# Kernel optimization log

Hardware: AMD Instinct MI355X
Metric: run time of the kernel (lower is better)

The kernel has to match this reference:

```python
import jax, jax.numpy as jnp
import numpy as np

N_NODES = 100000
N_EDGES = 3200000
IN_C, HID_C, OUT_C = 128, 64, 64


def setup_inputs() -> dict:
    key = jax.random.key(0)
    k = jax.random.split(key, 6)
    x = jax.random.normal(k[0], (N_NODES, IN_C), dtype=jnp.float32)
    edge_index = jax.random.randint(k[1], (2, N_EDGES), 0, N_NODES, dtype=jnp.int64)
    edge_weight = jax.random.uniform(k[2], (N_EDGES,), dtype=jnp.float32)
    W1 = jax.random.normal(k[3], (IN_C, HID_C), dtype=jnp.float32) * (1.0 / np.sqrt(IN_C))
    b1 = jnp.zeros((HID_C,), dtype=jnp.float32)
    W2 = jax.random.normal(k[4], (HID_C, OUT_C), dtype=jnp.float32) * (1.0 / np.sqrt(HID_C))
    b2 = jnp.zeros((OUT_C,), dtype=jnp.float32)
    return {"x": x, "edge_index": edge_index, "edge_weight": edge_weight,
            "W1": W1, "b1": b1, "W2": W2, "b2": b2}


def _gcn_norm(edge_index, edge_weight, num_nodes, dtype):
    # PyG GCNConv default: add self-loops (weight 1), symmetric normalization
    loop = jnp.arange(num_nodes, dtype=edge_index.dtype)
    row = jnp.concatenate([edge_index[0], loop])  # sources
    col = jnp.concatenate([edge_index[1], loop])  # targets (aggregation dim)
    w = jnp.concatenate([edge_weight.astype(dtype), jnp.ones((num_nodes,), dtype)])
    deg = jax.ops.segment_sum(w, col, num_segments=num_nodes)
    deg_inv_sqrt = jnp.where(deg > 0, jax.lax.rsqrt(deg), jnp.zeros((), dtype))
    norm = deg_inv_sqrt[row] * w * deg_inv_sqrt[col]
    return row, col, norm


def _gcn_conv(h, row, col, norm, W, b, num_nodes):
    h = h @ W                      # [N, C_out]
    msg = h[row] * norm[:, None]   # gather over sources, scale by edge norm
    out = jax.ops.segment_sum(msg, col, num_segments=num_nodes)  # scatter-add to targets
    return out + b


def reference(x, edge_index, edge_weight, W1, b1, W2, b2):
    num_nodes = x.shape[0]
    row, col, norm = _gcn_norm(edge_index, edge_weight, num_nodes, x.dtype)
    h = _gcn_conv(x, row, col, norm, W1, b1, num_nodes)
    h = jax.nn.relu(h)
    return _gcn_conv(h, row, col, norm, W2, b2, num_nodes)
```

## Files before the change

### kernel.cpp

```cpp
#include <hip/hip_runtime.h>
#include <hip/hip_bf16.h>

#define N_NODES 100000
#define N_EDGES 3200000
#define IN_C 128
#define HID_C 64
#define OUT_C 64

#define NBUCKET 196
#define SC_EDGES 4096
#define SC_PER   (SC_EDGES / 256)
#define SC_GRID  782
#define CAP 18432
#define MM1_GRID (N_NODES / 16)

struct EdgeRec { int s; float v; };

typedef float f32x2 __attribute__((ext_vector_type(2)));
typedef float f32x4 __attribute__((ext_vector_type(4)));
typedef short bf16x8 __attribute__((ext_vector_type(8)));
union F8 { uint4 u; bf16x8 f; };

__device__ __forceinline__ unsigned pack_bf16(float lo, float hi) {
    unsigned short l = __hip_bfloat16_raw(__float2bfloat16(lo)).x;
    unsigned short h = __hip_bfloat16_raw(__float2bfloat16(hi)).x;
    return ((unsigned)h << 16) | l;
}
__device__ __forceinline__ float bf_lo(unsigned u) {
    union { unsigned u; float f; } c; c.u = u << 16; return c.f;
}
__device__ __forceinline__ float bf_hi(unsigned u) {
    union { unsigned u; float f; } c; c.u = u & 0xffff0000u; return c.f;
}
__device__ __forceinline__ f32x2 bfp(unsigned u) {
    union { unsigned u; float f; } lo, hi;
    lo.u = u << 16; hi.u = u & 0xffff0000u;
    f32x2 r; r.x = lo.f; r.y = hi.f; return r;
}
__device__ __forceinline__ void pk_fma(f32x2& acc, f32x2 a, f32x2 w) {
    asm("v_pk_fma_f32 %0, %1, %2, %0" : "+v"(acc) : "v"(a), "v"(w));
}
__device__ __forceinline__ void edge_acc(f32x2* acc2, uint4 u, float w) {
    f32x2 wv; wv.x = w; wv.y = w;
    pk_fma(acc2[0], bfp(u.x), wv);
    pk_fma(acc2[1], bfp(u.y), wv);
    pk_fma(acc2[2], bfp(u.z), wv);
    pk_fma(acc2[3], bfp(u.w), wv);
}
__device__ __forceinline__ unsigned cvt_pk_bf16(float lo, float hi) {
    unsigned r;
    asm("v_cvt_pk_bf16_f32 %0, %1, %2" : "=v"(r) : "v"(lo), "v"(hi));
    return r;
}
__device__ __forceinline__ void split_frag(const float* f, uint4& hi4, uint4& lo4) {
    unsigned hi[4], lo[4];
    #pragma unroll
    for (int p = 0; p < 4; ++p) {
        hi[p] = cvt_pk_bf16(f[2 * p], f[2 * p + 1]);
        float r0 = f[2 * p]     - bf_lo(hi[p]);
        float r1 = f[2 * p + 1] - bf_hi(hi[p]);
        lo[p] = cvt_pk_bf16(r0, r1);
    }
    hi4 = make_uint4(hi[0], hi[1], hi[2], hi[3]);
    lo4 = make_uint4(lo[0], lo[1], lo[2], lo[3]);
}

__device__ __forceinline__ void scatter_body(const int* __restrict__ ei,
                                             const float* __restrict__ ew,
                                             int* __restrict__ gcursor,
                                             uint2* __restrict__ tmp,
                                             int* hist, int* scn, int* lcur,
                                             int* adj, uint2* rec,
                                             unsigned char* bk) {
    int tid = threadIdx.x;
    hist[tid] = 0;
    __syncthreads();
    int base = blockIdx.x * SC_EDGES;
    unsigned ys[SC_PER];
    float    ws[SC_PER];
    int      bs[SC_PER];
    for (int i = 0; i < SC_PER; ++i) {
        int e = base + i * 256 + tid;
        if (e < N_EDGES) {
            int t = ei[N_EDGES + e];
            bs[i] = t >> 9;
            ys[i] = (unsigned)ei[e] | ((unsigned)(t & 511) << 17);
            ws[i] = ew[e];
            atomicAdd(&hist[bs[i]], 1);
        } else bs[i] = -1;
    }
    __syncthreads();
    int v = hist[tid];
    scn[tid] = v;
    __syncthreads();
    for (int off = 1; off < 256; off <<= 1) {
        int t = scn[tid];
        int add = (tid >= off) ? scn[tid - off] : 0;
        __syncthreads();
        scn[tid] = t + add;
        __syncthreads();
    }
    int excl = scn[tid] - v;
    int gb = (v > 0) ? atomicAdd(&gcursor[tid], v) : 0;
    lcur[tid] = excl;
    adj[tid] = tid * CAP + gb - excl;
    __syncthreads();
    for (int i = 0; i < SC_PER; ++i) {
        if (bs[i] >= 0) {
            int j = atomicAdd(&lcur[bs[i]], 1);
            rec[j] = make_uint2(__float_as_uint(ws[i]), ys[i]);
            bk[j] = (unsigned char)bs[i];
        }
    }
    __syncthreads();
    int count = N_EDGES - base;
    if (count > SC_EDGES) count = SC_EDGES;
    for (int j = tid; j < count; j += 256) {
        int b = bk[j];
        tmp[adj[b] + j] = rec[j];
    }
}

template<int K>
__device__ __forceinline__ void mm_tile_bf(int tile,
                                           const float* __restrict__ X,
                                           const F8* bhi, const F8* blo,
                                           int lr, int kr, int col,
                                           unsigned* __restrict__ h) {
    constexpr int NKS = K / 32;
    int row0 = tile * 16;
    const float* xbase = X + (size_t)(row0 + lr) * K + kr * 8;
    float4 xa[NKS], xb[NKS];
    #pragma unroll
    for (int ks = 0; ks < NKS; ++ks) {
        const float4* xp = (const float4*)(xbase + ks * 32);
        xa[ks] = xp[0];
        xb[ks] = xp[1];
    }
    f32x4 acc = {0.f, 0.f, 0.f, 0.f};
    #pragma unroll
    for (int ks = 0; ks < NKS; ++ks) {
        float f[8] = {xa[ks].x, xa[ks].y, xa[ks].z, xa[ks].w,
                      xb[ks].x, xb[ks].y, xb[ks].z, xb[ks].w};
        F8 ahi, alo;
        split_frag(f, ahi.u, alo.u);
        acc = __builtin_amdgcn_mfma_f32_16x16x32_bf16(ahi.f, bhi[ks].f, acc, 0, 0, 0);
        acc = __builtin_amdgcn_mfma_f32_16x16x32_bf16(ahi.f, blo[ks].f, acc, 0, 0, 0);
        acc = __builtin_amdgcn_mfma_f32_16x16x32_bf16(alo.f, bhi[ks].f, acc, 0, 0, 0);
    }
    int rbase = row0 + kr * 4;
    float v0 = acc[0], v1 = acc[1], v2 = acc[2], v3 = acc[3];
    float o0 = __shfl_xor(v0, 1, 64);
    float o1 = __shfl_xor(v1, 1, 64);
    float o2 = __shfl_xor(v2, 1, 64);
    float o3 = __shfl_xor(v3, 1, 64);
    if ((lr & 1) == 0) {
        int ci = col >> 1;
        h[(rbase + 0) * 32 + ci] = pack_bf16(v0, o0);
        h[(rbase + 1) * 32 + ci] = pack_bf16(v1, o1);
        h[(rbase + 2) * 32 + ci] = pack_bf16(v2, o2);
        h[(rbase + 3) * 32 + ci] = pack_bf16(v3, o3);
    }
}

template<int K>
__device__ __forceinline__ void load_bfrags(const float* __restrict__ W,
                                            int kr, int col, F8* bhi, F8* blo) {
    #pragma unroll
    for (int ks = 0; ks < K / 32; ++ks) {
        const float* wp = W + (ks * 32 + kr * 8) * 64 + col;
        float f[8];
        #pragma unroll
        for (int j = 0; j < 8; ++j) f[j] = wp[j * 64];
        split_frag(f, bhi[ks].u, blo[ks].u);
    }
}

__global__ __launch_bounds__(256) void fused_scatter_mm1(const int* __restrict__ ei,
                                                         const float* __restrict__ ew,
                                                         int* __restrict__ gcursor,
                                                         uint2* __restrict__ tmp,
                                                         const float* __restrict__ x,
                                                         const float* __restrict__ W1,
                                                         unsigned* __restrict__ h) {
    __shared__ int hist[256];
    __shared__ int scn[256];
    __shared__ int lcur[256];
    __shared__ int adj[256];
    __shared__ uint2 rec[SC_EDGES];
    __shared__ unsigned char bk[SC_EDGES];
    if (blockIdx.x >= SC_GRID) {
        int l  = threadIdx.x & 63;
        int lr = l & 15;
        int kr = l >> 4;
        int col = (threadIdx.x >> 6) * 16 + lr;
        F8 bhi[IN_C / 32], blo[IN_C / 32];
        load_bfrags<IN_C>(W1, kr, col, bhi, blo);
        mm_tile_bf<IN_C>(blockIdx.x - SC_GRID, x, bhi, blo, lr, kr, col, h);
        return;
    }
    scatter_body(ei, ew, gcursor, tmp, hist, scn, lcur, adj, rec, bk);
}

template<int K>
__global__ __launch_bounds__(256) void mm_mfma_raw(const float* __restrict__ X,
                                                   const float* __restrict__ W,
                                                   unsigned* __restrict__ h) {
    int l  = threadIdx.x & 63;
    int lr = l & 15;
    int kr = l >> 4;
    int col = (threadIdx.x >> 6) * 16 + lr;
    F8 bhi[K / 32], blo[K / 32];
    load_bfrags<K>(W, kr, col, bhi, blo);
    for (int t = blockIdx.x; t < N_NODES / 16; t += gridDim.x)
        mm_tile_bf<K>(t, X, bhi, blo, lr, kr, col, h);
}

__global__ __launch_bounds__(512) void fine_sort(const int* __restrict__ gcursor,
                                                 const uint2* __restrict__ tmpPad,
                                                 int* __restrict__ rowptr,
                                                 float* __restrict__ dis,
                                                 EdgeRec* __restrict__ ed) {
    __shared__ int   cnt[512];
    __shared__ float wdeg[512];
    __shared__ int   s[512];
    __shared__ int   bsc[256];
    int tid = threadIdx.x;
    if (tid < 256) bsc[tid] = gcursor[tid];
    __syncthreads();
    for (int off = 1; off < 256; off <<= 1) {
        int t = (tid < 256) ? bsc[tid] : 0;
        int add = (tid < 256 && tid >= off) ? bsc[tid - off] : 0;
        __syncthreads();
        if (tid < 256) bsc[tid] = t + add;
        __syncthreads();
    }
    int bkt = blockIdx.x;
    int nEdge = gcursor[bkt];
    int bb = bsc[bkt] - nEdge;
    int nodeBase = bkt << 9;
    const uint2* tb = tmpPad + (size_t)bkt * CAP;
    cnt[tid] = 0;
    wdeg[tid] = 0.f;
    __syncthreads();
    for (int e = tid; e < nEdge; e += 512) {
        uint2 r = tb[e];
        int l = (r.y >> 17) & 511;
        atomicAdd(&cnt[l], 1);
        atomicAdd(&wdeg[l], __uint_as_float(r.x));
    }
    __syncthreads();
    int v = cnt[tid];
    s[tid] = v;
    __syncthreads();
    for (int off = 1; off < 512; off <<= 1) {
        int t = s[tid];
        int add = (tid >= off) ? s[tid - off] : 0;
        __syncthreads();
        s[tid] = t + add;
        __syncthreads();
    }
    int excl = s[tid] - v;
    int node = nodeBase + tid;
    if (node < N_NODES) {
        rowptr[node] = bb + excl;
        dis[node] = rsqrtf(wdeg[tid] + 1.0f);
    }
    if (node == N_NODES) rowptr[N_NODES] = N_EDGES;
    cnt[tid] = excl;
    __syncthreads();
    for (int e = tid; e < nEdge; e += 512) {
        uint2 r = tb[e];
        int l = (r.y >> 17) & 511;
        int p = atomicAdd(&cnt[l], 1);
        EdgeRec o;
        o.s = (int)(r.y & 0x1FFFFu);
        o.v = __uint_as_float(r.x);
        ed[bb + p] = o;
    }
}

__global__ __launch_bounds__(256, 8) void agg_kernel(const int* __restrict__ rowptr,
                                                     const EdgeRec* __restrict__ ed,
                                                     const unsigned* __restrict__ h,
                                                     const float* __restrict__ dis,
                                                     const float* __restrict__ b,
                                                     float* __restrict__ out,
                                                     int relu) {
    int node = blockIdx.x * 4 + (threadIdx.x >> 6);
    int lane = threadIdx.x & 63;
    int g = lane >> 3;
    int cl = lane & 7;
    int beg = rowptr[node];
    int end = rowptr[node + 1];
    const uint4* h16 = (const uint4*)h;
    const char*  hb  = (const char*)h + (size_t)cl * 16;
    float d  = dis[node];
    uint4 us = h16[(size_t)node * 8 + cl];
    f32x2 acc2[4];
    acc2[0] = 0.f; acc2[1] = 0.f; acc2[2] = 0.f; acc2[3] = 0.f;
    int n = end - beg;
    int nb = (n + 31) >> 5;
    int nm1 = n - 1;
    uint2 q0, q1, q2, q3;
    if (nb > 0) {
        q0 = *(const uint2*)(ed + beg + min(g,      nm1));
        q1 = *(const uint2*)(ed + beg + min(g + 8,  nm1));
        q2 = *(const uint2*)(ed + beg + min(g + 16, nm1));
        q3 = *(const uint2*)(ed + beg + min(g + 24, nm1));
        for (int bt = 0; bt < nb; ++bt) {
            int ob = (bt << 5) + g;
            float w0 = (ob      < n) ? __uint_as_float(q0.y) * dis[(int)q0.x] : 0.f;
            float w1 = (ob + 8  < n) ? __uint_as_float(q1.y) * dis[(int)q1.x] : 0.f;
            float w2 = (ob + 16 < n) ? __uint_as_float(q2.y) * dis[(int)q2.x] : 0.f;
            float w3 = (ob + 24 < n) ? __uint_as_float(q3.y) * dis[(int)q3.x] : 0.f;
            uint4 u0 = *(const uint4*)(hb + ((size_t)(unsigned)q0.x << 7));
            uint4 u1 = *(const uint4*)(hb + ((size_t)(unsigned)q1.x << 7));
            uint4 u2 = *(const uint4*)(hb + ((size_t)(unsigned)q2.x << 7));
            uint4 u3 = *(const uint4*)(hb + ((size_t)(unsigned)q3.x << 7));
            if (bt + 1 < nb) {
                int on = ob + 32;
                q0 = *(const uint2*)(ed + beg + min(on,      nm1));
                q1 = *(const uint2*)(ed + beg + min(on + 8,  nm1));
                q2 = *(const uint2*)(ed + beg + min(on + 16, nm1));
                q3 = *(const uint2*)(ed + beg + min(on + 24, nm1));
            }
            edge_acc(acc2, u0, w0);
            edge_acc(acc2, u1, w1);
            edge_acc(acc2, u2, w2);
            edge_acc(acc2, u3, w3);
        }
    }
    float acc[8] = { acc2[0].x, acc2[0].y, acc2[1].x, acc2[1].y,
                     acc2[2].x, acc2[2].y, acc2[3].x, acc2[3].y };
    #pragma unroll
    for (int kk = 0; kk < 8; ++kk) {
        acc[kk] += __shfl_xor(acc[kk], 8, 64);
        acc[kk] += __shfl_xor(acc[kk], 16, 64);
        acc[kk] += __shfl_xor(acc[kk], 32, 64);
    }
    if (g == 0) {
        float hs[8] = { bf_lo(us.x), bf_hi(us.x), bf_lo(us.y), bf_hi(us.y),
                        bf_lo(us.z), bf_hi(us.z), bf_lo(us.w), bf_hi(us.w) };
        const float4* b4 = (const float4*)b;
        float4 bv0 = b4[cl * 2], bv1 = b4[cl * 2 + 1];
        float4 v0, v1;
        v0.x = d * (acc[0] + d * hs[0]) + bv0.x;
        v0.y = d * (acc[1] + d * hs[1]) + bv0.y;
        v0.z = d * (acc[2] + d * hs[2]) + bv0.z;
        v0.w = d * (acc[3] + d * hs[3]) + bv0.w;
        v1.x = d * (acc[4] + d * hs[4]) + bv1.x;
        v1.y = d * (acc[5] + d * hs[5]) + bv1.y;
        v1.z = d * (acc[6] + d * hs[6]) + bv1.z;
        v1.w = d * (acc[7] + d * hs[7]) + bv1.w;
        if (relu) {
            v0.x = fmaxf(v0.x, 0.f); v0.y = fmaxf(v0.y, 0.f);
            v0.z = fmaxf(v0.z, 0.f); v0.w = fmaxf(v0.w, 0.f);
            v1.x = fmaxf(v1.x, 0.f); v1.y = fmaxf(v1.y, 0.f);
            v1.z = fmaxf(v1.z, 0.f); v1.w = fmaxf(v1.w, 0.f);
        }
        float4* o4 = (float4*)out;
        o4[node * 16 + cl * 2]     = v0;
        o4[node * 16 + cl * 2 + 1] = v1;
    }
}

extern "C" void kernel_launch(void* const* d_in, const int* in_sizes, int n_in,
                              void* d_out, int out_size, void* d_ws, size_t ws_size,
                              hipStream_t stream) {
    const float* x  = (const float*)d_in[0];
    const int*   ei = (const int*)d_in[1];
    const float* ew = (const float*)d_in[2];
    const float* W1 = (const float*)d_in[3];
    const float* b1 = (const float*)d_in[4];
    const float* W2 = (const float*)d_in[5];
    const float* b2 = (const float*)d_in[6];
    float* out = (float*)d_out;

    char* p = (char*)d_ws;
    auto carve = [&](size_t bytes) { char* r = p; p += (bytes + 255) & ~(size_t)255; return r; };
    int*      rowptr  = (int*)carve((N_NODES + 1) * 4);
    int*      gcursor = (int*)carve(256 * 4);
    float*    dis     = (float*)carve(N_NODES * 4);
    EdgeRec*  ed      = (EdgeRec*)carve((size_t)N_EDGES * 8);
    unsigned* h       = (unsigned*)carve((size_t)N_NODES * 64 * 2);
    size_t    tmpsz   = (size_t)NBUCKET * CAP * 8;
    size_t    asz     = (size_t)N_NODES * 64 * 4;
    char*     r2      = carve(tmpsz > asz ? tmpsz : asz);
    uint2*    tmpPad  = (uint2*)r2;
    float*    a       = (float*)r2;

    hipMemsetAsync(gcursor, 0, 256 * sizeof(int), stream);

    fused_scatter_mm1<<<SC_GRID + MM1_GRID, 256, 0, stream>>>(ei, ew, gcursor,
                                                              tmpPad, x, W1, h);
    fine_sort<<<NBUCKET, 512, 0, stream>>>(gcursor, tmpPad, rowptr, dis, ed);

    agg_kernel<<<N_NODES / 4, 256, 0, stream>>>(rowptr, ed, h, dis, b1, a, 1);

    mm_mfma_raw<HID_C><<<1250, 256, 0, stream>>>(a, W2, h);
    agg_kernel<<<N_NODES / 4, 256, 0, stream>>>(rowptr, ed, h, dis, b2, out, 0);
}
```

Measured before the change: 398.5 us.

## Split fine sort, prefold source norm into edges, pre-split layer-1 output to bf16

The fine sort is split into a count kernel and a place kernel. This lets the place step multiply each edge weight by the source node's inverse-sqrt degree once, so both aggregation passes drop the per-edge dis gather. The first aggregation now writes its output as hi/lo bf16 fragments, and a new single-tile MFMA kernel consumes them directly for the second matmul, which removes the fp32 intermediate and its conversion. In exchange there is an extra kernel launch and a second pass over the bucket temp data.

Result: faster. 363.6 us (-8.8%).

```diff
diff --git a/kernel.cpp b/kernel.cpp
--- a/kernel.cpp
+++ b/kernel.cpp
@@ -202,25 +202,10 @@
     scatter_body(ei, ew, gcursor, tmp, hist, scn, lcur, adj, rec, bk);
 }
 
-template<int K>
-__global__ __launch_bounds__(256) void mm_mfma_raw(const float* __restrict__ X,
-                                                   const float* __restrict__ W,
-                                                   unsigned* __restrict__ h) {
-    int l  = threadIdx.x & 63;
-    int lr = l & 15;
-    int kr = l >> 4;
-    int col = (threadIdx.x >> 6) * 16 + lr;
-    F8 bhi[K / 32], blo[K / 32];
-    load_bfrags<K>(W, kr, col, bhi, blo);
-    for (int t = blockIdx.x; t < N_NODES / 16; t += gridDim.x)
-        mm_tile_bf<K>(t, X, bhi, blo, lr, kr, col, h);
-}
-
-__global__ __launch_bounds__(512) void fine_sort(const int* __restrict__ gcursor,
-                                                 const uint2* __restrict__ tmpPad,
-                                                 int* __restrict__ rowptr,
-                                                 float* __restrict__ dis,
-                                                 EdgeRec* __restrict__ ed) {
+__global__ __launch_bounds__(512) void fine_count(const int* __restrict__ gcursor,
+                                                  const uint2* __restrict__ tmpPad,
+                                                  int* __restrict__ rowptr,
+                                                  float* __restrict__ dis) {
     __shared__ int   cnt[512];
     __shared__ float wdeg[512];
     __shared__ int   s[512];
@@ -267,15 +252,32 @@
         dis[node] = rsqrtf(wdeg[tid] + 1.0f);
     }
     if (node == N_NODES) rowptr[N_NODES] = N_EDGES;
-    cnt[tid] = excl;
+}
+
+__global__ __launch_bounds__(512) void fine_place(const uint2* __restrict__ tmpPad,
+                                                  const int* __restrict__ rowptr,
+                                                  const float* __restrict__ dis,
+                                                  EdgeRec* __restrict__ ed) {
+    __shared__ int cnt[512];
+    int tid = threadIdx.x;
+    int bkt = blockIdx.x;
+    int nodeBase = bkt << 9;
+    int bb = rowptr[nodeBase];
+    int endIdx = (bkt + 1) << 9;
+    if (endIdx > N_NODES) endIdx = N_NODES;
+    int nEdge = rowptr[endIdx] - bb;
+    const uint2* tb = tmpPad + (size_t)bkt * CAP;
+    int node = nodeBase + tid;
+    cnt[tid] = (node < N_NODES) ? rowptr[node] - bb : 0;
     __syncthreads();
     for (int e = tid; e < nEdge; e += 512) {
         uint2 r = tb[e];
         int l = (r.y >> 17) & 511;
+        int src = (int)(r.y & 0x1FFFFu);
         int p = atomicAdd(&cnt[l], 1);
         EdgeRec o;
-        o.s = (int)(r.y & 0x1FFFFu);
-        o.v = __uint_as_float(r.x);
+        o.s = src;
+        o.v = __uint_as_float(r.x) * dis[src];
         ed[bb + p] = o;
     }
 }
@@ -286,7 +288,7 @@
                                                      const float* __restrict__ dis,
                                                      const float* __restrict__ b,
                                                      float* __restrict__ out,
-                                                     int relu) {
+                                                     int relu, int packa) {
     int node = blockIdx.x * 4 + (threadIdx.x >> 6);
     int lane = threadIdx.x & 63;
     int g = lane >> 3;
@@ -310,10 +312,10 @@
         q3 = *(const uint2*)(ed + beg + min(g + 24, nm1));
         for (int bt = 0; bt < nb; ++bt) {
             int ob = (bt << 5) + g;
-            float w0 = (ob      < n) ? __uint_as_float(q0.y) * dis[(int)q0.x] : 0.f;
-            float w1 = (ob + 8  < n) ? __uint_as_float(q1.y) * dis[(int)q1.x] : 0.f;
-            float w2 = (ob + 16 < n) ? __uint_as_float(q2.y) * dis[(int)q2.x] : 0.f;
-            float w3 = (ob + 24 < n) ? __uint_as_float(q3.y) * dis[(int)q3.x] : 0.f;
+            float w0 = (ob      < n) ? __uint_as_float(q0.y) : 0.f;
+            float w1 = (ob + 8  < n) ? __uint_as_float(q1.y) : 0.f;
+            float w2 = (ob + 16 < n) ? __uint_as_float(q2.y) : 0.f;
+            float w3 = (ob + 24 < n) ? __uint_as_float(q3.y) : 0.f;
             uint4 u0 = *(const uint4*)(hb + ((size_t)(unsigned)q0.x << 7));
             uint4 u1 = *(const uint4*)(hb + ((size_t)(unsigned)q1.x << 7));
             uint4 u2 = *(const uint4*)(hb + ((size_t)(unsigned)q2.x << 7));
@@ -344,24 +346,71 @@
                         bf_lo(us.z), bf_hi(us.z), bf_lo(us.w), bf_hi(us.w) };
         const float4* b4 = (const float4*)b;
         float4 bv0 = b4[cl * 2], bv1 = b4[cl * 2 + 1];
-        float4 v0, v1;
-        v0.x = d * (acc[0] + d * hs[0]) + bv0.x;
-        v0.y = d * (acc[1] + d * hs[1]) + bv0.y;
-        v0.z = d * (acc[2] + d * hs[2]) + bv0.z;
-        v0.w = d * (acc[3] + d * hs[3]) + bv0.w;
-        v1.x = d * (acc[4] + d * hs[4]) + bv1.x;
-        v1.y = d * (acc[5] + d * hs[5]) + bv1.y;
-        v1.z = d * (acc[6] + d * hs[6]) + bv1.z;
-        v1.w = d * (acc[7] + d * hs[7]) + bv1.w;
+        float vv[8];
+        vv[0] = d * (acc[0] + d * hs[0]) + bv0.x;
+        vv[1] = d * (acc[1] + d * hs[1]) + bv0.y;
+        vv[2] = d * (acc[2] + d * hs[2]) + bv0.z;
+        vv[3] = d * (acc[3] + d * hs[3]) + bv0.w;
+        vv[4] = d * (acc[4] + d * hs[4]) + bv1.x;
+        vv[5] = d * (acc[5] + d * hs[5]) + bv1.y;
+        vv[6] = d * (acc[6] + d * hs[6]) + bv1.z;
+        vv[7] = d * (acc[7] + d * hs[7]) + bv1.w;
         if (relu) {
-            v0.x = fmaxf(v0.x, 0.f); v0.y = fmaxf(v0.y, 0.f);
-            v0.z = fmaxf(v0.z, 0.f); v0.w = fmaxf(v0.w, 0.f);
-            v1.x = fmaxf(v1.x, 0.f); v1.y = fmaxf(v1.y, 0.f);
-            v1.z = fmaxf(v1.z, 0.f); v1.w = fmaxf(v1.w, 0.f);
+            #pragma unroll
+            for (int kk = 0; kk < 8; ++kk) vv[kk] = fmaxf(vv[kk], 0.f);
         }
-        float4* o4 = (float4*)out;
-        o4[node * 16 + cl * 2]     = v0;
-        o4[node * 16 + cl * 2 + 1] = v1;
+        if (packa) {
+            uint4 hi4, lo4;
+            split_frag(vv, hi4, lo4);
+            uint4* ab = (uint4*)out;
+            ab[(size_t)node * 16 + cl]     = hi4;
+            ab[(size_t)node * 16 + 8 + cl] = lo4;
+        } else {
+            float4 v0, v1;
+            v0.x = vv[0]; v0.y = vv[1]; v0.z = vv[2]; v0.w = vv[3];
+            v1.x = vv[4]; v1.y = vv[5]; v1.z = vv[6]; v1.w = vv[7];
+            float4* o4 = (float4*)out;
+            o4[node * 16 + cl * 2]     = v0;
+            o4[node * 16 + cl * 2 + 1] = v1;
+        }
+    }
+}
+
+__global__ __launch_bounds__(256) void mm2_bf(const unsigned* __restrict__ A,
+                                              const float* __restrict__ W,
+                                              unsigned* __restrict__ h) {
+    int wv = threadIdx.x >> 6;
+    int l  = threadIdx.x & 63;
+    int lr = l & 15;
+    int kr = l >> 4;
+    int col = wv * 16 + lr;
+    int row0 = blockIdx.x * 16;
+    const uint4* a4 = (const uint4*)A;
+    size_t rb = (size_t)(row0 + lr) * 16;
+    F8 ah0, al0, ah1, al1;
+    ah0.u = a4[rb + kr];          al0.u = a4[rb + 8 + kr];
+    ah1.u = a4[rb + 4 + kr];      al1.u = a4[rb + 12 + kr];
+    F8 bhi[2], blo[2];
+    load_bfrags<HID_C>(W, kr, col, bhi, blo);
+    f32x4 acc = {0.f, 0.f, 0.f, 0.f};
+    acc = __builtin_amdgcn_mfma_f32_16x16x32_bf16(ah0.f, bhi[0].f, acc, 0, 0, 0);
+    acc = __builtin_amdgcn_mfma_f32_16x16x32_bf16(ah0.f, blo[0].f, acc, 0, 0, 0);
+    acc = __builtin_amdgcn_mfma_f32_16x16x32_bf16(al0.f, bhi[0].f, acc, 0, 0, 0);
+    acc = __builtin_amdgcn_mfma_f32_16x16x32_bf16(ah1.f, bhi[1].f, acc, 0, 0, 0);
+    acc = __builtin_amdgcn_mfma_f32_16x16x32_bf16(ah1.f, blo[1].f, acc, 0, 0, 0);
+    acc = __builtin_amdgcn_mfma_f32_16x16x32_bf16(al1.f, bhi[1].f, acc, 0, 0, 0);
+    int rbase = row0 + kr * 4;
+    float v0 = acc[0], v1 = acc[1], v2 = acc[2], v3 = acc[3];
+    float o0 = __shfl_xor(v0, 1, 64);
+    float o1 = __shfl_xor(v1, 1, 64);
+    float o2 = __shfl_xor(v2, 1, 64);
+    float o3 = __shfl_xor(v3, 1, 64);
+    if ((lr & 1) == 0) {
+        int ci = col >> 1;
+        h[(rbase + 0) * 32 + ci] = pack_bf16(v0, o0);
+        h[(rbase + 1) * 32 + ci] = pack_bf16(v1, o1);
+        h[(rbase + 2) * 32 + ci] = pack_bf16(v2, o2);
+        h[(rbase + 3) * 32 + ci] = pack_bf16(v3, o3);
     }
 }
 
@@ -385,19 +434,20 @@
     EdgeRec*  ed      = (EdgeRec*)carve((size_t)N_EDGES * 8);
     unsigned* h       = (unsigned*)carve((size_t)N_NODES * 64 * 2);
     size_t    tmpsz   = (size_t)NBUCKET * CAP * 8;
-    size_t    asz     = (size_t)N_NODES * 64 * 4;
+    size_t    asz     = (size_t)N_NODES * 256;
     char*     r2      = carve(tmpsz > asz ? tmpsz : asz);
     uint2*    tmpPad  = (uint2*)r2;
-    float*    a       = (float*)r2;
+    unsigned* a       = (unsigned*)r2;
 
     hipMemsetAsync(gcursor, 0, 256 * sizeof(int), stream);
 
     fused_scatter_mm1<<<SC_GRID + MM1_GRID, 256, 0, stream>>>(ei, ew, gcursor,
                                                               tmpPad, x, W1, h);
-    fine_sort<<<NBUCKET, 512, 0, stream>>>(gcursor, tmpPad, rowptr, dis, ed);
-
-    agg_kernel<<<N_NODES / 4, 256, 0, stream>>>(rowptr, ed, h, dis, b1, a, 1);
-
-    mm_mfma_raw<HID_C><<<1250, 256, 0, stream>>>(a, W2, h);
-    agg_kernel<<<N_NODES / 4, 256, 0, stream>>>(rowptr, ed, h, dis, b2, out, 0);
-}
+    fine_count<<<NBUCKET, 512, 0, stream>>>(gcursor, tmpPad, rowptr, dis);
+    fine_place<<<NBUCKET, 512, 0, stream>>>(tmpPad, rowptr, dis, ed);
+
+    agg_kernel<<<N_NODES / 4, 256, 0, stream>>>(rowptr, ed, h, dis, b1,
+                                                (float*)a, 1, 1);
+    mm2_bf<<<N_NODES / 16, 256, 0, stream>>>(a, W2, h);
+    agg_kernel<<<N_NODES / 4, 256, 0, stream>>>(rowptr, ed, h, dis, b2, out, 0, 0);
+}
```
